# Kernel optimization log

Hardware: AMD Instinct MI355X
Metric: run time of the kernel (lower is better)

Reference implementation:

```python
import jax, jax.numpy as jnp
import numpy as np

ALPHA = 0.2  # LeakyReLU negative slope
NEG_BIG = -9e15


def setup_inputs() -> dict:
    key = jax.random.key(0)
    k1, k2, k3, k4 = jax.random.split(key, 4)
    N, F_IN, F_OUT = 8192, 256, 128
    h = jax.random.normal(k1, (N, F_IN), dtype=jnp.float32)
    adj = jax.random.randint(k2, (N, N), 0, 2, dtype=jnp.int32)
    # xavier_uniform with gain=1.414
    def xavier(k, shape, gain=1.414):
        fan_in, fan_out = shape[0], shape[1]
        bound = gain * np.sqrt(6.0 / (fan_in + fan_out))
        return jax.random.uniform(k, shape, jnp.float32, -bound, bound)
    W = xavier(k3, (F_IN, F_OUT))
    a = xavier(k4, (2 * F_OUT, 1))
    return {"h": h, "adj": adj, "W": W, "a": a}


def reference(h, adj, W, a):
    # Wh: [N, F_out]
    Wh = h @ W
    F_out = W.shape[1]
    a1 = a[:F_out, 0]   # attends to source (row) node
    a2 = a[F_out:, 0]   # attends to target (col) node
    # Additive decomposition of concat([Wh_i, Wh_j]) @ a:
    # e[i, j] = leaky_relu(Wh_i . a1 + Wh_j . a2)
    f1 = Wh @ a1  # [N]
    f2 = Wh @ a2  # [N]
    e = jax.nn.leaky_relu(f1[:, None] + f2[None, :], negative_slope=ALPHA)  # [N, N]
    scores = jnp.where(adj > 0, e, jnp.float32(NEG_BIG))
    attention = jax.nn.softmax(scores, axis=1)
    # dropout is identity in eval mode (training=False)
    h_prime = attention @ Wh  # [N, F_out]
    return h_prime
```

## Files before the change

kernel.cpp:

```cpp
#include <hip/hip_runtime.h>


#define N_NODES 8192
#define F_IN 256
#define F_OUT 128
#define RPB 32
#define JCH 128
#define JSPLIT 2
#define JRANGE (N_NODES / JSPLIT)
#define NCH (JRANGE / JCH)

typedef _Float16 half8 __attribute__((ext_vector_type(8)));
typedef float floatx4 __attribute__((ext_vector_type(4)));
typedef float f32x4 __attribute__((ext_vector_type(4)));
typedef int i32x4 __attribute__((ext_vector_type(4)));

__device__ __align__(16) float g_Wh[N_NODES * F_OUT];
__device__ __align__(16) _Float16 g_WhT[(size_t)F_OUT * N_NODES];
__device__ __align__(16) float g_f1[N_NODES];
__device__ __align__(16) float g_f2[N_NODES];
__device__ __align__(16) float g_part[JSPLIT][N_NODES * F_OUT];
__device__ __align__(16) float g_spart[JSPLIT][N_NODES];

__global__ __launch_bounds__(256, 2) void wh_kernel(
    const float* __restrict__ h, const float* __restrict__ W) {
  __shared__ float hT[F_IN][20];
  const int t = threadIdx.x;
  const int i0 = blockIdx.x * 16;
  {
    const int row = t >> 4;
    const int fu = t & 15;
#pragma unroll
    for (int r = 0; r < 4; ++r) {
      const int ku = r * 16 + fu;
      const float4 v = *(const float4*)(h + (size_t)(i0 + row) * F_IN + ku * 4);
      hT[ku * 4 + 0][row] = v.x; hT[ku * 4 + 1][row] = v.y;
      hT[ku * 4 + 2][row] = v.z; hT[ku * 4 + 3][row] = v.w;
    }
  }
  __syncthreads();
  const int c = t & 127;
  const int rg = t >> 7;
  float acc[8];
#pragma unroll
  for (int r = 0; r < 8; ++r) acc[r] = 0.f;
#pragma unroll 8
  for (int k = 0; k < F_IN; ++k) {
    const float wv = W[k * F_OUT + c];
    const float4 x0 = *(const float4*)(&hT[k][rg * 8]);
    const float4 x1 = *(const float4*)(&hT[k][rg * 8 + 4]);
    acc[0] = fmaf(x0.x, wv, acc[0]); acc[1] = fmaf(x0.y, wv, acc[1]);
    acc[2] = fmaf(x0.z, wv, acc[2]); acc[3] = fmaf(x0.w, wv, acc[3]);
    acc[4] = fmaf(x1.x, wv, acc[4]); acc[5] = fmaf(x1.y, wv, acc[5]);
    acc[6] = fmaf(x1.z, wv, acc[6]); acc[7] = fmaf(x1.w, wv, acc[7]);
  }
#pragma unroll
  for (int r = 0; r < 8; ++r)
    g_Wh[(size_t)(i0 + rg * 8 + r) * F_OUT + c] = acc[r];
  union { _Float16 hh[8]; uint4 u4; } pk;
#pragma unroll
  for (int r = 0; r < 8; ++r) pk.hh[r] = (_Float16)acc[r];
  *(uint4*)(g_WhT + (size_t)c * N_NODES + i0 + rg * 8) = pk.u4;
}

__global__ __launch_bounds__(256) void f12_kernel(const float* __restrict__ a) {
  const int t = threadIdx.x;
  const int row = blockIdx.x * 2 + (t >> 7);
  const int c = t & 127;
  const float wh = g_Wh[(size_t)row * F_OUT + c];
  float p1 = wh * a[c];
  float p2 = wh * a[F_OUT + c];
  for (int o = 32; o > 0; o >>= 1) {
    p1 += __shfl_down(p1, o, 64);
    p2 += __shfl_down(p2, o, 64);
  }
  __shared__ float s1[4], s2[4];
  const int w = t >> 6;
  if ((t & 63) == 0) { s1[w] = p1; s2[w] = p2; }
  __syncthreads();
  if ((t & 127) == 0) {
    g_f1[row] = s1[w] + s1[w + 1];
    g_f2[row] = s2[w] + s2[w + 1];
  }
}

__device__ __forceinline__ float score_p(int a, float f2v, float f1r) {
  float s = f1r + f2v;
  s = fmaxf(s, 0.2f * s);
  float arg = (a > 0) ? fmaf(s, 1.44269504088896f, -16.0f) : -1.0e5f;
  return __builtin_amdgcn_exp2f(arg);
}

__global__ __launch_bounds__(256, 2) void gat_attn_kernel(const int* __restrict__ adj) {
  const int t = threadIdx.x;
  const int wave = t >> 6;
  const int lane = t & 63;
  const int mrow = lane & 15;
  const int quad = lane >> 4;
  const int i0 = blockIdx.x * RPB;
  const int js = blockIdx.y;
  const int jbase = js * JRANGE;
  const int jloc = wave * 32 + quad * 8;

  const float f1r0 = g_f1[i0 + mrow];
  const float f1r1 = g_f1[i0 + 16 + mrow];

  half8 ones;
#pragma unroll
  for (int e = 0; e < 8; ++e) ones[e] = (_Float16)1;

  floatx4 acc[2][8];
  floatx4 asum[2];
#pragma unroll
  for (int tl = 0; tl < 2; ++tl) {
    asum[tl] = (floatx4)0.f;
#pragma unroll
    for (int ct = 0; ct < 8; ++ct) acc[tl][ct] = (floatx4)0.f;
  }

  const int* ap0 = adj + (size_t)(i0 + mrow) * N_NODES + jbase + jloc;
  const int* ap1 = adj + (size_t)(i0 + 16 + mrow) * N_NODES + jbase + jloc;

  i32x4 A0[2][2], A1[2][2];
  f32x4 Fb[2][2];
  A0[0][0] = __builtin_nontemporal_load((const i32x4*)ap0);
  A0[0][1] = __builtin_nontemporal_load((const i32x4*)ap0 + 1);
  A1[0][0] = __builtin_nontemporal_load((const i32x4*)ap1);
  A1[0][1] = __builtin_nontemporal_load((const i32x4*)ap1 + 1);
  Fb[0][0] = *(const f32x4*)(g_f2 + jbase + jloc);
  Fb[0][1] = *(const f32x4*)(g_f2 + jbase + jloc + 4);

#pragma unroll 2
  for (int c = 0; c < NCH; ++c) {
    const int b = c & 1, nb = b ^ 1;
    const int jglob = jbase + c * JCH + jloc;

    half8 bfr[8];
#pragma unroll
    for (int ct = 0; ct < 8; ++ct)
      bfr[ct] = *(const half8*)(g_WhT + (size_t)(ct * 16 + mrow) * N_NODES + jglob);

    if (c + 1 < NCH) {
      A0[nb][0] = __builtin_nontemporal_load((const i32x4*)(ap0 + (c + 1) * JCH));
      A0[nb][1] = __builtin_nontemporal_load((const i32x4*)(ap0 + (c + 1) * JCH) + 1);
      A1[nb][0] = __builtin_nontemporal_load((const i32x4*)(ap1 + (c + 1) * JCH));
      A1[nb][1] = __builtin_nontemporal_load((const i32x4*)(ap1 + (c + 1) * JCH) + 1);
      Fb[nb][0] = *(const f32x4*)(g_f2 + jglob + JCH);
      Fb[nb][1] = *(const f32x4*)(g_f2 + jglob + JCH + 4);
    }

    half8 af0, af1;
#pragma unroll
    for (int e = 0; e < 4; ++e) {
      af0[e]     = (_Float16)score_p(A0[b][0][e], Fb[b][0][e], f1r0);
      af0[4 + e] = (_Float16)score_p(A0[b][1][e], Fb[b][1][e], f1r0);
      af1[e]     = (_Float16)score_p(A1[b][0][e], Fb[b][0][e], f1r1);
      af1[4 + e] = (_Float16)score_p(A1[b][1][e], Fb[b][1][e], f1r1);
    }

#pragma unroll
    for (int ct = 0; ct < 8; ++ct) {
      acc[0][ct] = __builtin_amdgcn_mfma_f32_16x16x32_f16(af0, bfr[ct], acc[0][ct], 0, 0, 0);
      acc[1][ct] = __builtin_amdgcn_mfma_f32_16x16x32_f16(af1, bfr[ct], acc[1][ct], 0, 0, 0);
    }
    asum[0] = __builtin_amdgcn_mfma_f32_16x16x32_f16(af0, ones, asum[0], 0, 0, 0);
    asum[1] = __builtin_amdgcn_mfma_f32_16x16x32_f16(af1, ones, asum[1], 0, 0, 0);
  }

  __shared__ float ldsO[RPB][F_OUT];
  __shared__ float ldsS[4][RPB];

  if (mrow == 0) {
#pragma unroll
    for (int tl = 0; tl < 2; ++tl)
#pragma unroll
      for (int r = 0; r < 4; ++r)
        ldsS[wave][tl * 16 + quad * 4 + r] = asum[tl][r];
  }
  for (int w = 0; w < 4; ++w) {
    if (wave == w) {
#pragma unroll
      for (int tl = 0; tl < 2; ++tl)
#pragma unroll
        for (int ct = 0; ct < 8; ++ct)
#pragma unroll
          for (int r = 0; r < 4; ++r) {
            float* p = &ldsO[tl * 16 + quad * 4 + r][ct * 16 + mrow];
            if (w == 0) *p = acc[tl][ct][r];
            else        *p += acc[tl][ct][r];
          }
    }
    __syncthreads();
  }
  {
    const int row = t >> 3;
    const int c0 = (t & 7) * 16;
    float* dst = g_part[js] + (size_t)(i0 + row) * F_OUT + c0;
#pragma unroll
    for (int q = 0; q < 4; ++q)
      *(f32x4*)(dst + q * 4) = *(const f32x4*)(&ldsO[row][c0 + q * 4]);
    if ((t & 7) == 0)
      g_spart[js][i0 + row] = ldsS[0][row] + ldsS[1][row] +
                              ldsS[2][row] + ldsS[3][row];
  }
}

__global__ __launch_bounds__(256) void comb_kernel(float* __restrict__ out) {
  const int u = blockIdx.x * 256 + threadIdx.x;
  const int row = u >> 5;
  const float s = g_spart[0][row] + g_spart[1][row];
  const f32x4 v = ((const f32x4*)g_part[0])[u] + ((const f32x4*)g_part[1])[u];
  ((f32x4*)out)[u] = v * (1.0f / s);
}

extern "C" void kernel_launch(void* const* d_in, const int* in_sizes, int n_in,
                              void* d_out, int out_size, void* d_ws, size_t ws_size,
                              hipStream_t stream) {
  const float* h = (const float*)d_in[0];
  const int* adj = (const int*)d_in[1];
  const float* W = (const float*)d_in[2];
  const float* a = (const float*)d_in[3];
  float* out = (float*)d_out;
  (void)d_ws; (void)ws_size;

  wh_kernel<<<dim3(N_NODES / 16), dim3(256), 0, stream>>>(h, W);
  f12_kernel<<<dim3(N_NODES / 2), dim3(256), 0, stream>>>(a);
  gat_attn_kernel<<<dim3(N_NODES / RPB, JSPLIT), dim3(256), 0, stream>>>(adj);
  comb_kernel<<<dim3(N_NODES * F_OUT / 4 / 256), dim3(256), 0, stream>>>(out);
}
```

Measured before the change: 456.3 us.

## Pack adjacency into a bitmask and raise the column split for attention

Adds a pre-pass that reads the int32 adjacency matrix once and packs it into 32-bit bitmasks with wave ballots. The attention kernel then reads compact mask words instead of 32 bytes of int per 8 entries, which cuts the main kernel's memory traffic. JSPLIT rises from 2 to 8 and the launch bound from 2 to 3 blocks per SM, and the explicit register double-buffering is dropped. The combine kernel now sums 8 partials, which adds partial-result traffic (8×4MB written and read) on top of the pack pass's full 256MB adjacency read.

```diff
diff --git a/kernel.cpp b/kernel.cpp
--- a/kernel.cpp
+++ b/kernel.cpp
@@ -6,21 +6,39 @@
 #define F_OUT 128
 #define RPB 32
 #define JCH 128
-#define JSPLIT 2
+#define JSPLIT 8
 #define JRANGE (N_NODES / JSPLIT)
 #define NCH (JRANGE / JCH)
+#define WPR (N_NODES / 32)
 
 typedef _Float16 half8 __attribute__((ext_vector_type(8)));
 typedef float floatx4 __attribute__((ext_vector_type(4)));
 typedef float f32x4 __attribute__((ext_vector_type(4)));
-typedef int i32x4 __attribute__((ext_vector_type(4)));
 
 __device__ __align__(16) float g_Wh[N_NODES * F_OUT];
 __device__ __align__(16) _Float16 g_WhT[(size_t)F_OUT * N_NODES];
 __device__ __align__(16) float g_f1[N_NODES];
 __device__ __align__(16) float g_f2[N_NODES];
+__device__ __align__(16) unsigned int g_mask[(size_t)N_NODES * WPR];
 __device__ __align__(16) float g_part[JSPLIT][N_NODES * F_OUT];
 __device__ __align__(16) float g_spart[JSPLIT][N_NODES];
+
+__global__ __launch_bounds__(256) void pack_kernel(const int* __restrict__ adj) {
+  const int row = blockIdx.x;
+  const int wv = threadIdx.x >> 6;
+  const int lane = threadIdx.x & 63;
+  __shared__ unsigned long long m[N_NODES / 64];
+  const int* arow = adj + (size_t)row * N_NODES;
+#pragma unroll 4
+  for (int it = 0; it < 32; ++it) {
+    const int j0 = (it * 4 + wv) * 64;
+    const int v = __builtin_nontemporal_load(arow + j0 + lane);
+    const unsigned long long b = __ballot(v > 0);
+    if (lane == 0) m[j0 >> 6] = b;
+  }
+  __syncthreads();
+  g_mask[(size_t)row * WPR + threadIdx.x] = ((const unsigned int*)m)[threadIdx.x];
+}
 
 __global__ __launch_bounds__(256, 2) void wh_kernel(
     const float* __restrict__ h, const float* __restrict__ W) {
@@ -84,14 +102,14 @@
   }
 }
 
-__device__ __forceinline__ float score_p(int a, float f2v, float f1r) {
+__device__ __forceinline__ float score_p(unsigned int bit, float f2v, float f1r) {
   float s = f1r + f2v;
   s = fmaxf(s, 0.2f * s);
-  float arg = (a > 0) ? fmaf(s, 1.44269504088896f, -16.0f) : -1.0e5f;
+  float arg = bit ? fmaf(s, 1.44269504088896f, -16.0f) : -1.0e5f;
   return __builtin_amdgcn_exp2f(arg);
 }
 
-__global__ __launch_bounds__(256, 2) void gat_attn_kernel(const int* __restrict__ adj) {
+__global__ __launch_bounds__(256, 3) void gat_attn_kernel() {
   const int t = threadIdx.x;
   const int wave = t >> 6;
   const int lane = t & 63;
@@ -101,6 +119,7 @@
   const int js = blockIdx.y;
   const int jbase = js * JRANGE;
   const int jloc = wave * 32 + quad * 8;
+  const int wb = jbase / 32 + wave;
 
   const float f1r0 = g_f1[i0 + mrow];
   const float f1r1 = g_f1[i0 + 16 + mrow];
@@ -118,44 +137,29 @@
     for (int ct = 0; ct < 8; ++ct) acc[tl][ct] = (floatx4)0.f;
   }
 
-  const int* ap0 = adj + (size_t)(i0 + mrow) * N_NODES + jbase + jloc;
-  const int* ap1 = adj + (size_t)(i0 + 16 + mrow) * N_NODES + jbase + jloc;
-
-  i32x4 A0[2][2], A1[2][2];
-  f32x4 Fb[2][2];
-  A0[0][0] = __builtin_nontemporal_load((const i32x4*)ap0);
-  A0[0][1] = __builtin_nontemporal_load((const i32x4*)ap0 + 1);
-  A1[0][0] = __builtin_nontemporal_load((const i32x4*)ap1);
-  A1[0][1] = __builtin_nontemporal_load((const i32x4*)ap1 + 1);
-  Fb[0][0] = *(const f32x4*)(g_f2 + jbase + jloc);
-  Fb[0][1] = *(const f32x4*)(g_f2 + jbase + jloc + 4);
-
-#pragma unroll 2
+  const unsigned int* mp0 = g_mask + (size_t)(i0 + mrow) * WPR + wb;
+  const unsigned int* mp1 = g_mask + (size_t)(i0 + 16 + mrow) * WPR + wb;
+
+#pragma unroll 1
   for (int c = 0; c < NCH; ++c) {
-    const int b = c & 1, nb = b ^ 1;
     const int jglob = jbase + c * JCH + jloc;
 
     half8 bfr[8];
 #pragma unroll
     for (int ct = 0; ct < 8; ++ct)
       bfr[ct] = *(const half8*)(g_WhT + (size_t)(ct * 16 + mrow) * N_NODES + jglob);
-
-    if (c + 1 < NCH) {
-      A0[nb][0] = __builtin_nontemporal_load((const i32x4*)(ap0 + (c + 1) * JCH));
-      A0[nb][1] = __builtin_nontemporal_load((const i32x4*)(ap0 + (c + 1) * JCH) + 1);
-      A1[nb][0] = __builtin_nontemporal_load((const i32x4*)(ap1 + (c + 1) * JCH));
-      A1[nb][1] = __builtin_nontemporal_load((const i32x4*)(ap1 + (c + 1) * JCH) + 1);
-      Fb[nb][0] = *(const f32x4*)(g_f2 + jglob + JCH);
-      Fb[nb][1] = *(const f32x4*)(g_f2 + jglob + JCH + 4);
-    }
+    const unsigned int m0 = mp0[c * 4];
+    const unsigned int m1 = mp1[c * 4];
+    const float4 F0 = *(const float4*)(g_f2 + jglob);
+    const float4 F1 = *(const float4*)(g_f2 + jglob + 4);
 
     half8 af0, af1;
 #pragma unroll
     for (int e = 0; e < 4; ++e) {
-      af0[e]     = (_Float16)score_p(A0[b][0][e], Fb[b][0][e], f1r0);
-      af0[4 + e] = (_Float16)score_p(A0[b][1][e], Fb[b][1][e], f1r0);
-      af1[e]     = (_Float16)score_p(A1[b][0][e], Fb[b][0][e], f1r1);
-      af1[4 + e] = (_Float16)score_p(A1[b][1][e], Fb[b][1][e], f1r1);
+      af0[e]     = (_Float16)score_p((m0 >> (quad * 8 + e)) & 1u,     F0[e], f1r0);
+      af0[4 + e] = (_Float16)score_p((m0 >> (quad * 8 + 4 + e)) & 1u, F1[e], f1r0);
+      af1[e]     = (_Float16)score_p((m1 >> (quad * 8 + e)) & 1u,     F0[e], f1r1);
+      af1[4 + e] = (_Float16)score_p((m1 >> (quad * 8 + 4 + e)) & 1u, F1[e], f1r1);
     }
 
 #pragma unroll
@@ -208,8 +212,13 @@
 __global__ __launch_bounds__(256) void comb_kernel(float* __restrict__ out) {
   const int u = blockIdx.x * 256 + threadIdx.x;
   const int row = u >> 5;
-  const float s = g_spart[0][row] + g_spart[1][row];
-  const f32x4 v = ((const f32x4*)g_part[0])[u] + ((const f32x4*)g_part[1])[u];
+  float s = 0.f;
+  f32x4 v = (f32x4)0.f;
+#pragma unroll
+  for (int p = 0; p < JSPLIT; ++p) {
+    s += g_spart[p][row];
+    v += ((const f32x4*)g_part[p])[u];
+  }
   ((f32x4*)out)[u] = v * (1.0f / s);
 }
 
@@ -223,8 +232,9 @@
   float* out = (float*)d_out;
   (void)d_ws; (void)ws_size;
 
+  pack_kernel<<<dim3(N_NODES), dim3(256), 0, stream>>>(adj);
   wh_kernel<<<dim3(N_NODES / 16), dim3(256), 0, stream>>>(h, W);
   f12_kernel<<<dim3(N_NODES / 2), dim3(256), 0, stream>>>(a);
-  gat_attn_kernel<<<dim3(N_NODES / RPB, JSPLIT), dim3(256), 0, stream>>>(adj);
+  gat_attn_kernel<<<dim3(N_NODES / RPB, JSPLIT), dim3(256), 0, stream>>>();
   comb_kernel<<<dim3(N_NODES * F_OUT / 4 / 256), dim3(256), 0, stream>>>(out);
 }
```

After: 506.2 us. 1.11x slower.
